# Kernel optimization log

Hardware: AMD Instinct MI355X
Metric: run time of the kernel (lower is better)

The kernel has to match this reference:

```python
import jax, jax.numpy as jnp
import numpy as np

D_MODEL = 1024
N_HEADS = 16
D_HEAD = D_MODEL // N_HEADS
WINDOW = 256
DILATION = 1
GLOBAL_IDX = (0,)
NEG_INF = float('-inf')


def longformer_mask(seq_len):
    # Vectorized version of the original O(S^2) Python-loop mask builder.
    i = jnp.arange(seq_len)[:, None]
    j = jnp.arange(seq_len)[None, :]
    d = jnp.abs(i - j)
    window_ok = (d <= WINDOW) & (d % DILATION == 0)  # includes diagonal (d==0)
    is_global = jnp.zeros((seq_len,), dtype=bool).at[jnp.array(GLOBAL_IDX)].set(True)
    global_ok = is_global[:, None] | is_global[None, :]
    return jnp.where(window_ok | global_ok, 0.0, NEG_INF).astype(jnp.float32)


def setup_inputs() -> dict:
    key = jax.random.key(0)
    ks = jax.random.split(key, 9)
    s = 1.0 / np.sqrt(D_MODEL)
    inp = {'x': jax.random.normal(ks[0], (2, 2048, D_MODEL), dtype=jnp.float32)}
    for n, kw, kb in (('q', ks[1], ks[2]), ('k', ks[3], ks[4]), ('v', ks[5], ks[6]), ('o', ks[7], ks[8])):
        inp['W' + n] = jax.random.uniform(kw, (D_MODEL, D_MODEL), jnp.float32, -s, s)
        inp['b' + n] = jax.random.uniform(kb, (D_MODEL,), jnp.float32, -s, s)
    return inp


def reference(x, Wq, bq, Wk, bk, Wv, bv, Wo, bo):
    B, S, _ = x.shape
    scale = D_HEAD ** -0.5

    def split_heads(t):  # [B,S,D] -> [B,H,S,d]
        return t.reshape(B, S, N_HEADS, D_HEAD).transpose(0, 2, 1, 3)

    Q = split_heads(x @ Wq + bq)
    K = split_heads(x @ Wk + bk)
    V = split_heads(x @ Wv + bv)

    scores = jnp.einsum('bhqd,bhkd->bhqk', Q, K) * scale
    scores = scores + longformer_mask(S)[None, None]
    attn = jax.nn.softmax(scores, axis=-1)  # dropout is identity in eval
    out = jnp.einsum('bhqk,bhkd->bhqd', attn, V)
    out = out.transpose(0, 2, 1, 3).reshape(B, S, D_MODEL)
    return out @ Wo + bo
```

## Files before the change

kernel.cpp:

```cpp
#include <hip/hip_runtime.h>
#include <hip/hip_bf16.h>

typedef __attribute__((ext_vector_type(8))) short short8;
typedef __attribute__((ext_vector_type(4))) float floatx4;
typedef __attribute__((ext_vector_type(8))) _Float16 half8;
typedef __attribute__((ext_vector_type(4))) _Float16 half4;
typedef __attribute__((ext_vector_type(2))) __fp16 fp16x2_raw;

using bf16 = __hip_bfloat16;
using fp16 = _Float16;

#define S_LEN 2048
#define DM 1024
#define NH 16
#define DH 64
#define WIN 256

__device__ __forceinline__ unsigned short f2b(float f) {
  __hip_bfloat16 h = __float2bfloat16(f);
  return *reinterpret_cast<unsigned short*>(&h);
}
__device__ __forceinline__ unsigned short f2h(float f) {
  fp16 h = (fp16)f;
  return *reinterpret_cast<unsigned short*>(&h);
}
__device__ __forceinline__ half4 pack4(float a, float b, float c, float d) {
  union { half4 h4; fp16x2_raw h2[2]; } u;
  u.h2[0] = __builtin_amdgcn_cvt_pkrtz(a, b);
  u.h2[1] = __builtin_amdgcn_cvt_pkrtz(c, d);
  return u.h4;
}
__device__ __forceinline__ void lds_load16(void* lds, const void* gptr) {
  __builtin_amdgcn_global_load_lds(
      (const __attribute__((address_space(1))) unsigned int*)gptr,
      (__attribute__((address_space(3))) unsigned int*)lds, 16, 0, 0);
}

__global__ __launch_bounds__(256) void k_prep(const float* __restrict__ x,
                                              const float* __restrict__ W0,
                                              const float* __restrict__ W1,
                                              const float* __restrict__ W2,
                                              const float* __restrict__ W3,
                                              bf16* __restrict__ wT,
                                              ushort4* __restrict__ xb) {
  const int tx = threadIdx.x, ty = threadIdx.y;
  if (blockIdx.z == 4) {
    const int tid = ty * 32 + tx;
    const int blk = blockIdx.y * 32 + blockIdx.x;
    const float4* in4 = (const float4*)x;
    #pragma unroll
    for (int k = 0; k < 4; ++k) {
      int i = k * 262144 + blk * 256 + tid;
      float4 v = in4[i];
      ushort4 o;
      o.x = f2b(v.x); o.y = f2b(v.y); o.z = f2b(v.z); o.w = f2b(v.w);
      xb[i] = o;
    }
    return;
  }
  __shared__ float t[32][33];
  const float* W = (blockIdx.z == 0) ? W0 : (blockIdx.z == 1) ? W1 : (blockIdx.z == 2) ? W2 : W3;
  bf16* O = wT + (size_t)blockIdx.z * 1024 * 1024;
  int x0 = blockIdx.x * 32, y0 = blockIdx.y * 32;
  #pragma unroll
  for (int i = 0; i < 32; i += 8) t[ty + i][tx] = W[(size_t)(y0 + ty + i) * 1024 + x0 + tx];
  __syncthreads();
  #pragma unroll
  for (int i = 0; i < 32; i += 8)
    O[(size_t)(x0 + ty + i) * 1024 + y0 + tx] = __float2bfloat16(t[tx][ty + i]);
}

__global__ __launch_bounds__(512) void k_qkv(const bf16* __restrict__ A,
                                             const bf16* __restrict__ Bt,
                                             const float* __restrict__ bias_q,
                                             const float* __restrict__ bias_k,
                                             const float* __restrict__ bias_v,
                                             fp16* __restrict__ Qh, fp16* __restrict__ Kh,
                                             fp16* __restrict__ Vt) {
  __shared__ __align__(16) char lds[131072];
  const int tid = threadIdx.x;
  const int wave = tid >> 6, lane = tid & 63;
  const int ln = lane & 15, quad = lane >> 4;
  const int wr = wave >> 2, wc = wave & 3;

  const int gi = blockIdx.x;
  const int wg = (gi & 7) * 24 + (gi >> 3);
  const int mt = wg / 12, nt = wg % 12;

  auto mkF = [](int p) {
    int q = p ^ (((p >> 9) & 1) << 5);
    int sub = q >> 10;
    int w = q & 1023;
    return (((sub >> 1) << 4) + (w >> 6)) * 2048 + (sub & 1) * 64 + (w & 63);
  };
  const int F0 = mkF(tid * 16);
  const int F1 = mkF(8192 + tid * 16);
  const char* Ab = (const char*)A + (size_t)mt * 524288;
  const char* Bb = (const char*)Bt + (size_t)nt * 524288;

  auto stg = [&](int region, const char* g) {
    lds_load16(lds + region + wave * 1024, g + F0);
    lds_load16(lds + region + 8192 + wave * 1024, g + F1);
  };

  stg(0, Ab);
  stg(16384, Ab + 262144);
  stg(32768, Bb);
  stg(49152, Bb + 262144);
  stg(65536, Ab + 128);
  stg(65536 + 16384, Ab + 262144 + 128);
  stg(65536 + 32768, Bb + 128);
  stg(65536 + 49152, Bb + 262144 + 128);

  floatx4 acc[8][4];
  #pragma unroll
  for (int i = 0; i < 8; ++i)
    #pragma unroll
    for (int j = 0; j < 4; ++j) acc[i][j] = (floatx4){0.f, 0.f, 0.f, 0.f};

  const int lnq = ln * 64 + ((quad * 16) ^ ((ln & 8) << 2));
  const int aoff = wr * 16384 + lnq;
  const int boff = 32768 + (wc >> 1) * 16384 + (wc & 1) * 8192 + lnq;

  asm volatile("s_waitcnt vmcnt(8)" ::: "memory");
  __builtin_amdgcn_s_barrier();

  for (int t = 0; t < 16; ++t) {
    const char* bb = lds + ((t & 1) << 16);
    const int sreg = (t & 1) << 16;
    const char* gA = Ab + (t + 2) * 128;
    const char* gB = Bb + (t + 2) * 128;
    const bool pf = (t + 2 < 16);

    short8 a0[4][2], b0[4][2];
    #pragma unroll
    for (int m2 = 0; m2 < 4; ++m2)
      #pragma unroll
      for (int kk = 0; kk < 2; ++kk)
        a0[m2][kk] = *(const short8*)(bb + aoff + m2 * 2048 + kk * 1024);
    #pragma unroll
    for (int n2 = 0; n2 < 2; ++n2)
      #pragma unroll
      for (int kk = 0; kk < 2; ++kk)
        b0[n2][kk] = *(const short8*)(bb + boff + n2 * 2048 + kk * 1024);
    __builtin_amdgcn_s_barrier();
    __builtin_amdgcn_s_setprio(1);
    #pragma unroll
    for (int m2 = 0; m2 < 4; ++m2)
      #pragma unroll
      for (int n2 = 0; n2 < 2; ++n2) {
        acc[m2][n2] = __builtin_amdgcn_mfma_f32_16x16x32_bf16(a0[m2][0], b0[n2][0], acc[m2][n2], 0, 0, 0);
        acc[m2][n2] = __builtin_amdgcn_mfma_f32_16x16x32_bf16(a0[m2][1], b0[n2][1], acc[m2][n2], 0, 0, 0);
      }
    __builtin_amdgcn_s_setprio(0);
    __builtin_amdgcn_s_barrier();

    #pragma unroll
    for (int n2 = 2; n2 < 4; ++n2)
      #pragma unroll
      for (int kk = 0; kk < 2; ++kk)
        b0[n2][kk] = *(const short8*)(bb + boff + n2 * 2048 + kk * 1024);
    __builtin_amdgcn_s_barrier();
    __builtin_amdgcn_s_setprio(1);
    #pragma unroll
    for (int m2 = 0; m2 < 4; ++m2)
      #pragma unroll
      for (int n2 = 2; n2 < 4; ++n2) {
        acc[m2][n2] = __builtin_amdgcn_mfma_f32_16x16x32_bf16(a0[m2][0], b0[n2][0], acc[m2][n2], 0, 0, 0);
        acc[m2][n2] = __builtin_amdgcn_mfma_f32_16x16x32_bf16(a0[m2][1], b0[n2][1], acc[m2][n2], 0, 0, 0);
      }
    __builtin_amdgcn_s_setprio(0);
    __builtin_amdgcn_s_barrier();

    short8 a1[4][2];
    #pragma unroll
    for (int m2 = 0; m2 < 4; ++m2)
      #pragma unroll
      for (int kk = 0; kk < 2; ++kk)
        a1[m2][kk] = *(const short8*)(bb + aoff + (4 + m2) * 2048 + kk * 1024);
    if (pf) {
      stg(sreg + 32768, gB);
      stg(sreg + 49152, gB + 262144);
    }
    __builtin_amdgcn_s_barrier();
    __builtin_amdgcn_s_setprio(1);
    #pragma unroll
    for (int m2 = 0; m2 < 4; ++m2)
      #pragma unroll
      for (int n2 = 0; n2 < 2; ++n2) {
        acc[4 + m2][n2] = __builtin_amdgcn_mfma_f32_16x16x32_bf16(a1[m2][0], b0[n2][0], acc[4 + m2][n2], 0, 0, 0);
        acc[4 + m2][n2] = __builtin_amdgcn_mfma_f32_16x16x32_bf16(a1[m2][1], b0[n2][1], acc[4 + m2][n2], 0, 0, 0);
      }
    __builtin_amdgcn_s_setprio(0);
    __builtin_amdgcn_s_barrier();

    if (pf) {
      stg(sreg, gA);
      stg(sreg + 16384, gA + 262144);
      asm volatile("s_waitcnt vmcnt(8)" ::: "memory");
    } else {
      asm volatile("s_waitcnt vmcnt(0)" ::: "memory");
    }
    __builtin_amdgcn_s_barrier();
    __builtin_amdgcn_s_setprio(1);
    #pragma unroll
    for (int m2 = 0; m2 < 4; ++m2)
      #pragma unroll
      for (int n2 = 2; n2 < 4; ++n2) {
        acc[4 + m2][n2] = __builtin_amdgcn_mfma_f32_16x16x32_bf16(a1[m2][0], b0[n2][0], acc[4 + m2][n2], 0, 0, 0);
        acc[4 + m2][n2] = __builtin_amdgcn_mfma_f32_16x16x32_bf16(a1[m2][1], b0[n2][1], acc[4 + m2][n2], 0, 0, 0);
      }
    __builtin_amdgcn_s_setprio(0);
    __builtin_amdgcn_s_barrier();
  }

  const int g = nt >> 2;
  if (g == 2) {
    #pragma unroll
    for (int ni = 0; ni < 4; ++ni) {
      int nn = (nt & 3) * 256 + wc * 64 + ni * 16 + ln;
      int h = nn >> 6, dd = nn & 63;
      float bias = bias_v[nn];
      #pragma unroll
      for (int mi = 0; mi < 8; ++mi) {
        int m = mt * 256 + wr * 128 + mi * 16 + quad * 4;
        int b = m >> 11, s = m & 2047;
        ushort4 pk;
        pk.x = f2h(acc[mi][ni][0] + bias);
        pk.y = f2h(acc[mi][ni][1] + bias);
        pk.z = f2h(acc[mi][ni][2] + bias);
        pk.w = f2h(acc[mi][ni][3] + bias);
        *(ushort4*)&Vt[((size_t)((b * NH + h) * DH + dd)) * S_LEN + s] = pk;
      }
    }
  } else {
    const float* bp = (g == 0) ? bias_q : bias_k;
    fp16* og = (g == 0) ? Qh : Kh;
    #pragma unroll
    for (int ni = 0; ni < 4; ++ni) {
      int nn = (nt & 3) * 256 + wc * 64 + ni * 16 + ln;
      int h = nn >> 6, dd = nn & 63;
      float bias = bp[nn];
      #pragma unroll
      for (int mi = 0; mi < 8; ++mi) {
        #pragma unroll
        for (int r = 0; r < 4; ++r) {
          int m = mt * 256 + wr * 128 + mi * 16 + quad * 4 + r;
          int b = m >> 11, s = m & 2047;
          og[(size_t)((b * NH + h) * S_LEN + s) * DH + dd] = (fp16)(acc[mi][ni][r] + bias);
        }
      }
    }
  }
}

template <int MODE>
__global__ __launch_bounds__(256) void k_gemm(const bf16* __restrict__ A,
                                              const bf16* __restrict__ Bt,
                                              const float* __restrict__ bias_q,
                                              const float* __restrict__ bias_k,
                                              const float* __restrict__ bias_v,
                                              fp16* __restrict__ Qh, fp16* __restrict__ Kh,
                                              fp16* __restrict__ Vt, float* __restrict__ outF) {
  __shared__ __align__(16) bf16 As[2][128 * 32];
  __shared__ __align__(16) bf16 Bs[2][128 * 32];
  const int tid = threadIdx.x;
  const int wave = tid >> 6, lane = tid & 63;
  const int gi = blockIdx.x;
  const int xcd = gi & 7, grr = gi >> 3;
  const int m0 = (xcd * 4 + (grr & 3)) * 128;
  const int n0 = (grr >> 2) * 128;
  const int r0 = tid >> 2;
  const int cb = (tid & 3) * 16;
  const char* Ag = (const char*)A + (size_t)(m0 + r0) * 2048 + cb;
  const char* Bg = (const char*)Bt + (size_t)(n0 + r0) * 2048 + cb;
  char* As0W = (char*)&As[0][0] + wave * 1024;
  char* As1W = (char*)&As[1][0] + wave * 1024;
  char* Bs0W = (char*)&Bs[0][0] + wave * 1024;
  char* Bs1W = (char*)&Bs[1][0] + wave * 1024;
  const int wm = (wave & 1) * 64, wn = (wave >> 1) * 64;
  const int ln = lane & 15, quad = lane >> 4;

  floatx4 acc[4][4];
  #pragma unroll
  for (int i = 0; i < 4; i++)
    #pragma unroll
    for (int j = 0; j < 4; j++) acc[i][j] = (floatx4){0.f, 0.f, 0.f, 0.f};

  for (int k0 = 0; k0 < 1024; k0 += 64) {
    __syncthreads();
    lds_load16(As0W,        Ag + k0 * 2);
    lds_load16(As0W + 4096, Ag + 64 * 2048 + k0 * 2);
    lds_load16(As1W,        Ag + k0 * 2 + 64);
    lds_load16(As1W + 4096, Ag + 64 * 2048 + k0 * 2 + 64);
    lds_load16(Bs0W,        Bg + k0 * 2);
    lds_load16(Bs0W + 4096, Bg + 64 * 2048 + k0 * 2);
    lds_load16(Bs1W,        Bg + k0 * 2 + 64);
    lds_load16(Bs1W + 4096, Bg + 64 * 2048 + k0 * 2 + 64);
    __syncthreads();
    short8 af0[4], af1[4], bf0[4], bf1[4];
    #pragma unroll
    for (int mi = 0; mi < 4; mi++) {
      af0[mi] = *(const short8*)&As[0][(wm + mi * 16 + ln) * 32 + quad * 8];
      af1[mi] = *(const short8*)&As[1][(wm + mi * 16 + ln) * 32 + quad * 8];
    }
    #pragma unroll
    for (int ni = 0; ni < 4; ni++) {
      bf0[ni] = *(const short8*)&Bs[0][(wn + ni * 16 + ln) * 32 + quad * 8];
      bf1[ni] = *(const short8*)&Bs[1][(wn + ni * 16 + ln) * 32 + quad * 8];
    }
    #pragma unroll
    for (int mi = 0; mi < 4; mi++)
      #pragma unroll
      for (int ni = 0; ni < 4; ni++) {
        acc[mi][ni] = __builtin_amdgcn_mfma_f32_16x16x32_bf16(af0[mi], bf0[ni], acc[mi][ni], 0, 0, 0);
        acc[mi][ni] = __builtin_amdgcn_mfma_f32_16x16x32_bf16(af1[mi], bf1[ni], acc[mi][ni], 0, 0, 0);
      }
  }

  if constexpr (MODE == 0) {
    #pragma unroll
    for (int ni = 0; ni < 4; ni++) {
      int n = n0 + wn + ni * 16 + ln;
      int g = n >> 10, nn = n & 1023;
      int h = nn >> 6, dd = nn & 63;
      if (g == 2) {
        float bias = bias_v[nn];
        #pragma unroll
        for (int mi = 0; mi < 4; mi++) {
          int m = m0 + wm + mi * 16 + quad * 4;
          int b = m >> 11, s = m & 2047;
          ushort4 pk;
          pk.x = f2h(acc[mi][ni][0] + bias);
          pk.y = f2h(acc[mi][ni][1] + bias);
          pk.z = f2h(acc[mi][ni][2] + bias);
          pk.w = f2h(acc[mi][ni][3] + bias);
          *(ushort4*)&Vt[((size_t)(b * NH + h) * DH + dd) * S_LEN + s] = pk;
        }
      } else {
        const float* bp = (g == 0) ? bias_q : bias_k;
        fp16* og = (g == 0) ? Qh : Kh;
        float bias = bp[nn];
        #pragma unroll
        for (int mi = 0; mi < 4; mi++) {
          #pragma unroll
          for (int r = 0; r < 4; r++) {
            int m = m0 + wm + mi * 16 + quad * 4 + r;
            int b = m >> 11, s = m & 2047;
            og[(size_t)((b * NH + h) * S_LEN + s) * DH + dd] = (fp16)(acc[mi][ni][r] + bias);
          }
        }
      }
    }
  } else {
    #pragma unroll
    for (int ni = 0; ni < 4; ni++) {
      int n = n0 + wn + ni * 16 + ln;
      float bias = bias_q[n];
      #pragma unroll
      for (int mi = 0; mi < 4; mi++)
        #pragma unroll
        for (int r = 0; r < 4; r++) {
          int m = m0 + wm + mi * 16 + quad * 4 + r;
          outF[(size_t)m * 1024 + n] = acc[mi][ni][r] + bias;
        }
    }
  }
}

__global__ __launch_bounds__(512, 4) void k_attn(const fp16* __restrict__ Qh,
                                                 const fp16* __restrict__ Kh,
                                                 const fp16* __restrict__ Vt,
                                                 bf16* __restrict__ aout) {
  __shared__ __align__(16) fp16 KsL[2][64 * 72];
  __shared__ __align__(16) fp16 VsL[2][64 * 72];

  const int i = blockIdx.x;
  const int xcd = i & 7, rr = i >> 3;
  const int bh = xcd * 4 + (rr & 3);
  const int tile = rr >> 2;
  const int b = bh >> 4, h = bh & 15;
  const size_t base = (size_t)bh * S_LEN * DH;
  const fp16* Qp = Qh + base;
  const fp16* Kp = Kh + base;
  const fp16* Vp = Vt + base;
  const float SC2 = 0.18033688011112042f;
  const int tid = threadIdx.x;

  const int w = tid >> 6, lane = tid & 63;
  const int ln = lane & 15, quad = lane >> 4;
  const int qb = tile * 128;
  const int qw = qb + w * 16;

  const half8 bq0 = *(const half8*)(Qp + (size_t)(qw + ln) * DH + quad * 8);
  const half8 bq1 = *(const half8*)(Qp + (size_t)(qw + ln) * DH + 32 + quad * 8);

  floatx4 acc[4];
  float l_i;

  {
    const half8 k0a = *(const half8*)(Kp + quad * 8);
    const half8 k0b = *(const half8*)(Kp + 32 + quad * 8);
    float s0 = 0.f;
    #pragma unroll
    for (int e = 0; e < 8; ++e)
      s0 += (float)bq0[e] * (float)k0a[e] + (float)bq1[e] * (float)k0b[e];
    s0 += __shfl_xor(s0, 16, 64);
    s0 += __shfl_xor(s0, 32, 64);
    float p0 = exp2f(fmaf(s0, SC2, -8.f));
    l_i = (quad == 0) ? p0 : 0.f;
    #pragma unroll
    for (int dt = 0; dt < 4; ++dt)
      #pragma unroll
      for (int r = 0; r < 4; ++r)
        acc[dt][r] = p0 * (float)Vp[(size_t)(dt * 16 + quad * 4 + r) * S_LEN];
  }

  int cs = qb - WIN; if (cs < 0) cs = 0;
  int ce = qb + 128 + WIN; if (ce > S_LEN) ce = S_LEN;

  const int rs = tid >> 3, cls = (tid & 7) * 8;

  uint4 kreg, vreg;
  auto stage_load = [&](int c) {
    kreg = *(const uint4*)(Kp + (size_t)(c + rs) * DH + cls);
    vreg = *(const uint4*)(Vp + (size_t)rs * S_LEN + c + cls);
  };
  auto stage_write = [&](int buf) {
    *(uint4*)&KsL[buf][rs * 72 + cls] = kreg;
    *(uint4*)&VsL[buf][rs * 72 + cls] = vreg;
  };

  auto compute = [&](int c, int buf) {
    floatx4 s[4];
    #pragma unroll
    for (int jt = 0; jt < 4; ++jt) {
      half8 k0 = *(const half8*)&KsL[buf][(jt * 16 + ln) * 72 + quad * 8];
      half8 k1 = *(const half8*)&KsL[buf][(jt * 16 + ln) * 72 + 32 + quad * 8];
      floatx4 z = (floatx4){0.f, 0.f, 0.f, 0.f};
      z = __builtin_amdgcn_mfma_f32_16x16x32_f16(k0, bq0, z, 0, 0, 0);
      s[jt] = __builtin_amdgcn_mfma_f32_16x16x32_f16(k1, bq1, z, 0, 0, 0);
    }
    half4 v01[8];
    #pragma unroll
    for (int dt = 0; dt < 2; ++dt)
      #pragma unroll
      for (int jt = 0; jt < 4; ++jt)
        v01[dt * 4 + jt] =
            *(const half4*)&VsL[buf][(dt * 16 + ln) * 72 + jt * 16 + quad * 4];
    const bool full_in = (c != 0) && (c >= qw - 241) && (c <= qw + 193);
    half4 Pt[4];
    if (full_in) {
      #pragma unroll
      for (int jt = 0; jt < 4; ++jt) {
        float p0 = exp2f(fmaf(s[jt][0], SC2, -8.f));
        float p1 = exp2f(fmaf(s[jt][1], SC2, -8.f));
        float p2 = exp2f(fmaf(s[jt][2], SC2, -8.f));
        float p3 = exp2f(fmaf(s[jt][3], SC2, -8.f));
        Pt[jt] = pack4(p0, p1, p2, p3);
        l_i += (p0 + p1) + (p2 + p3);
      }
    } else {
      const int q = qw + ln;
      #pragma unroll
      for (int jt = 0; jt < 4; ++jt) {
        float pv[4];
        #pragma unroll
        for (int r = 0; r < 4; ++r) {
          int j = c + jt * 16 + quad * 4 + r;
          int dq = q - j;
          bool ok = (dq <= WIN && dq >= -WIN) && (j != 0);
          pv[r] = ok ? exp2f(fmaf(s[jt][r], SC2, -8.f)) : 0.f;
        }
        Pt[jt] = pack4(pv[0], pv[1], pv[2], pv[3]);
        l_i += (pv[0] + pv[1]) + (pv[2] + pv[3]);
      }
    }
    half4 v23[8];
    #pragma unroll
    for (int dt = 0; dt < 2; ++dt)
      #pragma unroll
      for (int jt = 0; jt < 4; ++jt)
        v23[dt * 4 + jt] =
            *(const half4*)&VsL[buf][((dt + 2) * 16 + ln) * 72 + jt * 16 + quad * 4];
    #pragma unroll
    for (int jt = 0; jt < 4; ++jt) {
      acc[0] = __builtin_amdgcn_mfma_f32_16x16x16f16(v01[jt], Pt[jt], acc[0], 0, 0, 0);
      acc[1] = __builtin_amdgcn_mfma_f32_16x16x16f16(v01[4 + jt], Pt[jt], acc[1], 0, 0, 0);
    }
    #pragma unroll
    for (int jt = 0; jt < 4; ++jt) {
      acc[2] = __builtin_amdgcn_mfma_f32_16x16x16f16(v23[jt], Pt[jt], acc[2], 0, 0, 0);
      acc[3] = __builtin_amdgcn_mfma_f32_16x16x16f16(v23[4 + jt], Pt[jt], acc[3], 0, 0, 0);
    }
  };

  stage_load(cs);
  stage_write(0);
  __syncthreads();
  int buf = 0;
  for (int c = cs; c < ce; c += 64) {
    const bool hasnext = (c + 64 < ce);
    if (hasnext) stage_load(c + 64);
    compute(c, buf);
    if (hasnext) stage_write(buf ^ 1);
    __syncthreads();
    buf ^= 1;
  }

  {
    float lt = l_i;
    lt += __shfl_xor(lt, 16, 64);
    lt += __shfl_xor(lt, 32, 64);
    const float inv = 1.0f / lt;
    const int q = qw + ln;
    if (q != 0) {
      #pragma unroll
      for (int dt = 0; dt < 4; ++dt) {
        ushort4 pk;
        pk.x = f2b(acc[dt][0] * inv);
        pk.y = f2b(acc[dt][1] * inv);
        pk.z = f2b(acc[dt][2] * inv);
        pk.w = f2b(acc[dt][3] * inv);
        *(ushort4*)&aout[(size_t)(b * S_LEN + q) * DM + h * DH + dt * 16 + quad * 4] = pk;
      }
    }
  }

  if (tile == 0) {
    float* sP = (float*)&KsL[0][0];
    float* oR = (float*)&VsL[0][0];
    float* red = (float*)&VsL[1][0];
    const int g2 = lane >> 3, e8 = lane & 7;
    const half8 q0t = *(const half8*)(Qp + e8 * 8);
    float lsum = 0.f;
    for (int it = 0; it < 32; ++it) {
      int grp = w * 32 + it;
      const half8 kv = *(const half8*)(Kp + (size_t)(grp * 8 + g2) * DH + e8 * 8);
      float p = 0.f;
      #pragma unroll
      for (int e = 0; e < 8; ++e) p += (float)q0t[e] * (float)kv[e];
      p += __shfl_xor(p, 1, 64);
      p += __shfl_xor(p, 2, 64);
      p += __shfl_xor(p, 4, 64);
      p = exp2f(fmaf(p, SC2, -8.f));
      if (e8 == 0) sP[grp * 8 + g2] = p;
      lsum += p;
    }
    #pragma unroll
    for (int off = 1; off < 64; off <<= 1) lsum += __shfl_xor(lsum, off, 64);
    if (lane == 0) red[w] = lsum;
    __syncthreads();
    const float ltot = (red[0] + red[1] + red[2] + red[3] +
                        red[4] + red[5] + red[6] + red[7]) * 0.125f;
    const int d = tid & 63, qu = tid >> 6;
    float o = 0.f;
    for (int j0 = qu * 256; j0 < qu * 256 + 256; j0 += 8) {
      half8 vv = *(const half8*)(Vp + (size_t)d * S_LEN + j0);
      #pragma unroll
      for (int e = 0; e < 8; ++e) o += sP[j0 + e] * (float)vv[e];
    }
    oR[tid] = o;
    __syncthreads();
    if (tid < 64) {
      float oo = oR[tid] + oR[tid + 64] + oR[tid + 128] + oR[tid + 192] +
                 oR[tid + 256] + oR[tid + 320] + oR[tid + 384] + oR[tid + 448];
      aout[(size_t)(b * S_LEN) * DM + h * DH + tid] = __float2bfloat16(oo / ltot);
    }
  }
}

extern "C" void kernel_launch(void* const* d_in, const int* in_sizes, int n_in,
                              void* d_out, int out_size, void* d_ws, size_t ws_size,
                              hipStream_t stream) {
  const float* x  = (const float*)d_in[0];
  const float* Wq = (const float*)d_in[1];
  const float* bq = (const float*)d_in[2];
  const float* Wk = (const float*)d_in[3];
  const float* bk = (const float*)d_in[4];
  const float* Wv = (const float*)d_in[5];
  const float* bv = (const float*)d_in[6];
  const float* Wo = (const float*)d_in[7];
  const float* bo = (const float*)d_in[8];
  float* out = (float*)d_out;

  const size_t SEG = (size_t)4096 * 1024;
  bf16* xb = (bf16*)d_ws;
  bf16* wT = xb + SEG;
  fp16* Qh = (fp16*)(wT + SEG);
  fp16* Kh = Qh + SEG;
  fp16* Vt = Kh + SEG;
  bf16* ao = (bf16*)(Vt + SEG);

  k_prep<<<dim3(32, 32, 5), dim3(32, 8), 0, stream>>>(x, Wq, Wk, Wv, Wo, wT, (ushort4*)xb);
  k_qkv<<<dim3(192), dim3(512), 0, stream>>>(xb, wT, bq, bk, bv, Qh, Kh, Vt);
  k_attn<<<dim3(512), dim3(512), 0, stream>>>(Qh, Kh, Vt, ao);
  k_gemm<1><<<dim3(256), dim3(256), 0, stream>>>(ao, wT + (size_t)3 * 1024 * 1024, bo,
                                                 nullptr, nullptr, nullptr, nullptr, nullptr, out);
}
```

Before: 185.8 us.

## Restructure QKV GEMM main loop into finer-grained staggered LDS prefetch schedule

The K loop of the QKV projection GEMM is unrolled by two and the global-to-LDS staging is reordered. Each A/B half-tile load is now issued between individual MFMA sub-blocks, and A for the next step is loaded into the buffer being consumed once its reads finish. The aim is to keep fewer loads in flight per wait (vmcnt 4 instead of 8) while spreading memory traffic more evenly across the compute phases. The risk is that the tighter buffer reuse depends on the barrier ordering for correctness, and the extra lgkmcnt waits may add stalls.

```diff
diff --git a/kernel.cpp b/kernel.cpp
--- a/kernel.cpp
+++ b/kernel.cpp
@@ -103,12 +103,10 @@
     lds_load16(lds + region + 8192 + wave * 1024, g + F1);
   };
 
-  stg(0, Ab);
-  stg(16384, Ab + 262144);
   stg(32768, Bb);
   stg(49152, Bb + 262144);
-  stg(65536, Ab + 128);
-  stg(65536 + 16384, Ab + 262144 + 128);
+  stg(0,     Ab);
+  stg(16384, Ab + 262144);
   stg(65536 + 32768, Bb + 128);
   stg(65536 + 49152, Bb + 262144 + 128);
 
@@ -122,96 +120,78 @@
   const int aoff = wr * 16384 + lnq;
   const int boff = 32768 + (wc >> 1) * 16384 + (wc & 1) * 8192 + lnq;
 
-  asm volatile("s_waitcnt vmcnt(8)" ::: "memory");
-  __builtin_amdgcn_s_barrier();
-
-  for (int t = 0; t < 16; ++t) {
-    const char* bb = lds + ((t & 1) << 16);
-    const int sreg = (t & 1) << 16;
-    const char* gA = Ab + (t + 2) * 128;
-    const char* gB = Bb + (t + 2) * 128;
-    const bool pf = (t + 2 < 16);
-
-    short8 a0[4][2], b0[4][2];
+  auto RDA = [&](const char* bb, int mb, short8 (&a)[4][2]) {
     #pragma unroll
     for (int m2 = 0; m2 < 4; ++m2)
       #pragma unroll
       for (int kk = 0; kk < 2; ++kk)
-        a0[m2][kk] = *(const short8*)(bb + aoff + m2 * 2048 + kk * 1024);
-    #pragma unroll
-    for (int n2 = 0; n2 < 2; ++n2)
+        a[m2][kk] = *(const short8*)(bb + aoff + (mb + m2) * 2048 + kk * 1024);
+  };
+  auto RDB = [&](const char* bb, int nb, short8 (&b)[4][2]) {
+    #pragma unroll
+    for (int n2 = nb; n2 < nb + 2; ++n2)
       #pragma unroll
       for (int kk = 0; kk < 2; ++kk)
-        b0[n2][kk] = *(const short8*)(bb + boff + n2 * 2048 + kk * 1024);
+        b[n2][kk] = *(const short8*)(bb + boff + n2 * 2048 + kk * 1024);
+  };
+  auto MM = [&](int mb, int nb, short8 (&a)[4][2], short8 (&b)[4][2]) {
     __builtin_amdgcn_s_barrier();
+    asm volatile("s_waitcnt lgkmcnt(0)" ::: "memory");
     __builtin_amdgcn_s_setprio(1);
     #pragma unroll
     for (int m2 = 0; m2 < 4; ++m2)
       #pragma unroll
-      for (int n2 = 0; n2 < 2; ++n2) {
-        acc[m2][n2] = __builtin_amdgcn_mfma_f32_16x16x32_bf16(a0[m2][0], b0[n2][0], acc[m2][n2], 0, 0, 0);
-        acc[m2][n2] = __builtin_amdgcn_mfma_f32_16x16x32_bf16(a0[m2][1], b0[n2][1], acc[m2][n2], 0, 0, 0);
+      for (int n2 = nb; n2 < nb + 2; ++n2) {
+        acc[mb + m2][n2] = __builtin_amdgcn_mfma_f32_16x16x32_bf16(a[m2][0], b[n2][0], acc[mb + m2][n2], 0, 0, 0);
+        acc[mb + m2][n2] = __builtin_amdgcn_mfma_f32_16x16x32_bf16(a[m2][1], b[n2][1], acc[mb + m2][n2], 0, 0, 0);
       }
     __builtin_amdgcn_s_setprio(0);
     __builtin_amdgcn_s_barrier();
-
-    #pragma unroll
-    for (int n2 = 2; n2 < 4; ++n2)
-      #pragma unroll
-      for (int kk = 0; kk < 2; ++kk)
-        b0[n2][kk] = *(const short8*)(bb + boff + n2 * 2048 + kk * 1024);
-    __builtin_amdgcn_s_barrier();
-    __builtin_amdgcn_s_setprio(1);
-    #pragma unroll
-    for (int m2 = 0; m2 < 4; ++m2)
-      #pragma unroll
-      for (int n2 = 2; n2 < 4; ++n2) {
-        acc[m2][n2] = __builtin_amdgcn_mfma_f32_16x16x32_bf16(a0[m2][0], b0[n2][0], acc[m2][n2], 0, 0, 0);
-        acc[m2][n2] = __builtin_amdgcn_mfma_f32_16x16x32_bf16(a0[m2][1], b0[n2][1], acc[m2][n2], 0, 0, 0);
-      }
-    __builtin_amdgcn_s_setprio(0);
-    __builtin_amdgcn_s_barrier();
-
-    short8 a1[4][2];
-    #pragma unroll
-    for (int m2 = 0; m2 < 4; ++m2)
-      #pragma unroll
-      for (int kk = 0; kk < 2; ++kk)
-        a1[m2][kk] = *(const short8*)(bb + aoff + (4 + m2) * 2048 + kk * 1024);
+  };
+
+  asm volatile("s_waitcnt vmcnt(4)" ::: "memory");
+  __builtin_amdgcn_s_barrier();
+
+  for (int i = 0; i < 8; ++i) {
+    const char* bu = lds;
+    const char* bv = lds + 65536;
+    const int o1 = (2 * i + 1) * 128, o2 = (2 * i + 2) * 128, o3 = (2 * i + 3) * 128;
+    const bool pf = (i < 7);
+    short8 a0[4][2], a1[4][2], b0[4][2];
+
+    RDA(bu, 0, a0); RDB(bu, 0, b0);
+    stg(65536 + 0, Ab + o1);
+    MM(0, 0, a0, b0);
+    RDB(bu, 2, b0);
+    stg(65536 + 16384, Ab + 262144 + o1);
+    MM(0, 2, a0, b0);
+    RDA(bu, 4, a1);
+    if (pf) stg(32768, Bb + o2);
+    MM(4, 0, a1, b0);
     if (pf) {
-      stg(sreg + 32768, gB);
-      stg(sreg + 49152, gB + 262144);
-    }
-    __builtin_amdgcn_s_barrier();
-    __builtin_amdgcn_s_setprio(1);
-    #pragma unroll
-    for (int m2 = 0; m2 < 4; ++m2)
-      #pragma unroll
-      for (int n2 = 0; n2 < 2; ++n2) {
-        acc[4 + m2][n2] = __builtin_amdgcn_mfma_f32_16x16x32_bf16(a1[m2][0], b0[n2][0], acc[4 + m2][n2], 0, 0, 0);
-        acc[4 + m2][n2] = __builtin_amdgcn_mfma_f32_16x16x32_bf16(a1[m2][1], b0[n2][1], acc[4 + m2][n2], 0, 0, 0);
-      }
-    __builtin_amdgcn_s_setprio(0);
-    __builtin_amdgcn_s_barrier();
-
-    if (pf) {
-      stg(sreg, gA);
-      stg(sreg + 16384, gA + 262144);
-      asm volatile("s_waitcnt vmcnt(8)" ::: "memory");
+      stg(49152, Bb + 262144 + o2);
+      asm volatile("s_waitcnt vmcnt(4)" ::: "memory");
     } else {
       asm volatile("s_waitcnt vmcnt(0)" ::: "memory");
     }
-    __builtin_amdgcn_s_barrier();
-    __builtin_amdgcn_s_setprio(1);
-    #pragma unroll
-    for (int m2 = 0; m2 < 4; ++m2)
-      #pragma unroll
-      for (int n2 = 2; n2 < 4; ++n2) {
-        acc[4 + m2][n2] = __builtin_amdgcn_mfma_f32_16x16x32_bf16(a1[m2][0], b0[n2][0], acc[4 + m2][n2], 0, 0, 0);
-        acc[4 + m2][n2] = __builtin_amdgcn_mfma_f32_16x16x32_bf16(a1[m2][1], b0[n2][1], acc[4 + m2][n2], 0, 0, 0);
-      }
-    __builtin_amdgcn_s_setprio(0);
-    __builtin_amdgcn_s_barrier();
+    MM(4, 2, a1, b0);
+
+    RDA(bv, 0, a0); RDB(bv, 0, b0);
+    if (pf) stg(0, Ab + o2);
+    MM(0, 0, a0, b0);
+    RDB(bv, 2, b0);
+    if (pf) stg(16384, Ab + 262144 + o2);
+    MM(0, 2, a0, b0);
+    RDA(bv, 4, a1);
+    if (pf) stg(65536 + 32768, Bb + o3);
+    MM(4, 0, a1, b0);
+    if (pf) {
+      stg(65536 + 49152, Bb + 262144 + o3);
+      asm volatile("s_waitcnt vmcnt(4)" ::: "memory");
+    } else {
+      asm volatile("s_waitcnt vmcnt(0)" ::: "memory");
+    }
+    MM(4, 2, a1, b0);
   }
 
   const int g = nt >> 2;
```

Result: no change. 182.2 us (-1.9%).
